# Kernel tuning notes

Hardware: AMD Instinct MI355X
Metric: run time of the kernel (lower is better)

Reference implementation:

```python
import jax, jax.numpy as jnp
import numpy as np

B = 128
NCOL, NCOND = 128, 16
C = NCOL * NCOND          # 2048 channels
NRODT = 512               # groups
D = C // NRODT            # 4 channels per group (tree depth)
NEST = 128                # n_estimator
NFOREST = 100
NHEAD = 1
NHID = 128
EPS = 1e-5


def group_norm(x, w, b, groups, eps=EPS):
    # x: [B, C]; torch GroupNorm (biased variance over each group's channels)
    Bn, Cn = x.shape
    xg = x.reshape(Bn, groups, Cn // groups)
    mu = xg.mean(-1, keepdims=True)
    var = xg.var(-1, keepdims=True)
    xn = ((xg - mu) * jax.lax.rsqrt(var + eps)).reshape(Bn, Cn)
    return xn * w + b


def setup_inputs() -> dict:
    key = jax.random.key(0)
    ks = jax.random.split(key, 11)
    O = jax.random.normal(ks[0], (B, C, 1), jnp.float32)
    gn1_w = jax.random.normal(ks[1], (C,), jnp.float32) * 0.1 + 1.0
    gn1_b = jax.random.normal(ks[2], (C,), jnp.float32) * 0.1
    W1 = jax.random.normal(ks[3], (NRODT, D, D), jnp.float32) * 0.3
    b1 = jax.random.normal(ks[4], (NRODT, D), jnp.float32) * 0.1
    gn2_w = jax.random.normal(ks[5], (C,), jnp.float32) * 0.1 + 1.0
    gn2_b = jax.random.normal(ks[6], (C,), jnp.float32) * 0.1
    W2 = jax.random.normal(ks[7], (NRODT, D, NHEAD), jnp.float32) * 0.3
    b2 = jax.random.normal(ks[8], (NRODT, NHEAD), jnp.float32) * 0.1
    E = jax.random.normal(ks[9], (NRODT, NHID), jnp.float32)
    # eval-mode fixed sample_without_replacement: argsort of uniform, take first NEST
    swr = jnp.argsort(jax.random.uniform(ks[10], (NFOREST, NRODT)), axis=-1)[:, :NEST]
    return {"O": O, "gn1_w": gn1_w, "gn1_b": gn1_b, "W1": W1, "b1": b1,
            "gn2_w": gn2_w, "gn2_b": gn2_b, "W2": W2, "b2": b2, "E": E,
            "swr": swr}


def reference(O, gn1_w, gn1_b, W1, b1, gn2_w, gn2_b, W2, b2, E, swr):
    b = O.shape[0]
    x = O[..., 0]                                    # [B, C]
    # phi_2: GN -> grouped 1x1 conv (per-group DxD matmul) -> ReLU -> GN -> grouped conv to NHEAD
    x = group_norm(x, gn1_w, gn1_b, NRODT)
    x = x.reshape(b, NRODT, D)
    x = jnp.einsum('bgd,gde->bge', x, W1) + b1       # [B, NRODT, D]
    x = jax.nn.relu(x).reshape(b, C)
    x = group_norm(x, gn2_w, gn2_b, NRODT)
    x = x.reshape(b, NRODT, D)
    w = jnp.einsum('bgd,gdh->bgh', x, W2) + b2       # [B, NRODT, NHEAD]
    # gather -> softmax over estimators -> weighted embedding combine
    w_prime = jax.nn.softmax(w[:, swr], axis=-2)[..., None]   # [B, F, EST, H, 1]
    E_prime = E[swr].reshape(1, NFOREST, NEST, NHEAD, NHID // NHEAD)
    F = (w_prime * E_prime).sum(-3).reshape(b, NFOREST, NHID)  # [B, F, NHID]
    return F
```

## Files before the change

### kernel.cpp

```cpp
#include <hip/hip_runtime.h>

#define BB     128
#define CCH    2048
#define NRODT  512
#define NEST   128
#define NF     100
#define NHID   128
#define BT     32
#define TPB    512

typedef __attribute__((ext_vector_type(8))) short short8v;
typedef __attribute__((ext_vector_type(4))) float f32x4;

static __device__ __forceinline__ unsigned short f2bf(float x) {
    unsigned u = __float_as_uint(x);
    u += 0x7FFFu + ((u >> 16) & 1u);
    return (unsigned short)(u >> 16);
}
static __device__ __forceinline__ float bf2f(unsigned short h) {
    return __uint_as_float(((unsigned)h) << 16);
}

__global__ __launch_bounds__(256) void phi2_kernel(
    const float* __restrict__ O,
    const float* __restrict__ g1w, const float* __restrict__ g1b,
    const float* __restrict__ W1,  const float* __restrict__ b1,
    const float* __restrict__ g2w, const float* __restrict__ g2b,
    const float* __restrict__ W2,  const float* __restrict__ b2,
    const float* __restrict__ E,
    float* __restrict__ wbuf,
    unsigned* __restrict__ Esp)
{
    const int t = blockIdx.x * 256 + threadIdx.x;
    const int b = t >> 9;
    const int g = t & (NRODT - 1);

    {
        const float ex = E[t];
        const unsigned short xh = f2bf(ex);
        const float r = ex - bf2f(xh);
        const unsigned short xl = f2bf(r);
        Esp[t] = ((unsigned)xh) | (((unsigned)xl) << 16);
    }

    const float4 x = *reinterpret_cast<const float4*>(O + (size_t)b * CCH + g * 4);

    float m  = 0.25f * ((x.x + x.y) + (x.z + x.w));
    float d0 = x.x - m, d1 = x.y - m, d2 = x.z - m, d3 = x.w - m;
    float v  = 0.25f * ((d0 * d0 + d1 * d1) + (d2 * d2 + d3 * d3));
    float iv = rsqrtf(v + 1e-5f);
    const float4 gw1 = *reinterpret_cast<const float4*>(g1w + g * 4);
    const float4 gb1 = *reinterpret_cast<const float4*>(g1b + g * 4);
    float a0 = fmaf(d0 * iv, gw1.x, gb1.x);
    float a1 = fmaf(d1 * iv, gw1.y, gb1.y);
    float a2 = fmaf(d2 * iv, gw1.z, gb1.z);
    float a3 = fmaf(d3 * iv, gw1.w, gb1.w);

    const float4 r0 = *reinterpret_cast<const float4*>(W1 + g * 16 + 0);
    const float4 r1 = *reinterpret_cast<const float4*>(W1 + g * 16 + 4);
    const float4 r2 = *reinterpret_cast<const float4*>(W1 + g * 16 + 8);
    const float4 r3 = *reinterpret_cast<const float4*>(W1 + g * 16 + 12);
    const float4 bc = *reinterpret_cast<const float4*>(b1 + g * 4);
    float y0 = fmaf(a0, r0.x, fmaf(a1, r1.x, fmaf(a2, r2.x, fmaf(a3, r3.x, bc.x))));
    float y1 = fmaf(a0, r0.y, fmaf(a1, r1.y, fmaf(a2, r2.y, fmaf(a3, r3.y, bc.y))));
    float y2 = fmaf(a0, r0.z, fmaf(a1, r1.z, fmaf(a2, r2.z, fmaf(a3, r3.z, bc.z))));
    float y3 = fmaf(a0, r0.w, fmaf(a1, r1.w, fmaf(a2, r2.w, fmaf(a3, r3.w, bc.w))));
    y0 = fmaxf(y0, 0.f); y1 = fmaxf(y1, 0.f); y2 = fmaxf(y2, 0.f); y3 = fmaxf(y3, 0.f);

    m  = 0.25f * ((y0 + y1) + (y2 + y3));
    d0 = y0 - m; d1 = y1 - m; d2 = y2 - m; d3 = y3 - m;
    v  = 0.25f * ((d0 * d0 + d1 * d1) + (d2 * d2 + d3 * d3));
    iv = rsqrtf(v + 1e-5f);
    const float4 gw2 = *reinterpret_cast<const float4*>(g2w + g * 4);
    const float4 gb2 = *reinterpret_cast<const float4*>(g2b + g * 4);
    float z0 = fmaf(d0 * iv, gw2.x, gb2.x);
    float z1 = fmaf(d1 * iv, gw2.y, gb2.y);
    float z2 = fmaf(d2 * iv, gw2.z, gb2.z);
    float z3 = fmaf(d3 * iv, gw2.w, gb2.w);

    const float4 w2 = *reinterpret_cast<const float4*>(W2 + g * 4);
    float res = fmaf(z0, w2.x, fmaf(z1, w2.y, fmaf(z2, w2.z, fmaf(z3, w2.w, b2[g]))));

    wbuf[g * BB + b] = res;
}

__global__ __launch_bounds__(TPB) void forest_mfma_kernel(
    const float*    __restrict__ wv,
    const unsigned* __restrict__ Esp,
    const int*      __restrict__ swr,
    float* __restrict__ out)
{
    __shared__ __align__(16) short Prow[BT][136];
    __shared__ __align__(16) char  pool[2 * 128 * 72 * 2];
    __shared__ int   ids[NEST];
    __shared__ float invs[BT];

    short (*Ehi)[72] = reinterpret_cast<short(*)[72]>(pool);
    short (*Elo)[72] = reinterpret_cast<short(*)[72]>(pool + 128 * 72 * 2);
    float (*wT)[36]  = reinterpret_cast<float(*)[36]>(pool);

    const int f   = blockIdx.x;
    const int b0  = blockIdx.y * BT;
    const int tid = threadIdx.x;

    if (tid < NEST) ids[tid] = swr[f * NEST + tid];
    __syncthreads();

    {
        const int e = tid >> 2;
        const int j = tid & 3;
        const float* src = wv + (size_t)ids[e] * BB + b0 + (j << 3);
        const float4 va = *reinterpret_cast<const float4*>(src);
        const float4 vb = *reinterpret_cast<const float4*>(src + 4);
        *reinterpret_cast<float4*>(&wT[e][(j << 3) + 0]) = va;
        *reinterpret_cast<float4*>(&wT[e][(j << 3) + 4]) = vb;
    }
    __syncthreads();

    {
        const int bl = tid >> 4;
        const int jj = tid & 15;
        float val[8];
        float mx = -3.4e38f;
        #pragma unroll
        for (int k = 0; k < 8; ++k) {
            val[k] = wT[jj + (k << 4)][bl];
            mx = fmaxf(mx, val[k]);
        }
        mx = fmaxf(mx, __shfl_xor(mx, 1));
        mx = fmaxf(mx, __shfl_xor(mx, 2));
        mx = fmaxf(mx, __shfl_xor(mx, 4));
        mx = fmaxf(mx, __shfl_xor(mx, 8));
        float sum = 0.f;
        #pragma unroll
        for (int k = 0; k < 8; ++k) {
            float ex = __expf(val[k] - mx);
            sum += ex;
            Prow[bl][jj + (k << 4)] = (short)f2bf(ex);
        }
        sum += __shfl_xor(sum, 1);
        sum += __shfl_xor(sum, 2);
        sum += __shfl_xor(sum, 4);
        sum += __shfl_xor(sum, 8);
        if (jj == 0) invs[bl] = 1.f / sum;
    }
    __syncthreads();

    const int lane = tid & 63;
    const int wid  = tid >> 6;
    const int rt   = wid & 1;
    const int ct0  = (wid >> 1) << 1;
    const int lm   = lane & 15;
    const int lk   = (lane >> 4) << 3;

    f32x4 acc0 = {0.f, 0.f, 0.f, 0.f};
    f32x4 acc1 = {0.f, 0.f, 0.f, 0.f};

    const int h  = tid & 127;
    const int eg = tid >> 7;

    #pragma unroll
    for (int hf = 0; hf < 2; ++hf) {
        {
            short hbuf[16], lbuf[16];
            #pragma unroll
            for (int i = 0; i < 16; ++i) {
                const int row = ids[hf * 64 + eg * 16 + i];
                const unsigned v = Esp[(size_t)row * NHID + h];
                hbuf[i] = (short)(v & 0xFFFFu);
                lbuf[i] = (short)(v >> 16);
            }
            if (hf == 1) __syncthreads();
            *reinterpret_cast<short8v*>(&Ehi[h][eg * 16 + 0]) = *reinterpret_cast<short8v*>(&hbuf[0]);
            *reinterpret_cast<short8v*>(&Ehi[h][eg * 16 + 8]) = *reinterpret_cast<short8v*>(&hbuf[8]);
            *reinterpret_cast<short8v*>(&Elo[h][eg * 16 + 0]) = *reinterpret_cast<short8v*>(&lbuf[0]);
            *reinterpret_cast<short8v*>(&Elo[h][eg * 16 + 8]) = *reinterpret_cast<short8v*>(&lbuf[8]);
        }
        __syncthreads();

        #pragma unroll
        for (int kbl = 0; kbl < 2; ++kbl) {
            const short8v a =
                *reinterpret_cast<const short8v*>(&Prow[rt * 16 + lm][(hf * 2 + kbl) * 32 + lk]);
            const short8v bh0 = *reinterpret_cast<const short8v*>(&Ehi[ct0 * 16 + lm][kbl * 32 + lk]);
            const short8v bl0 = *reinterpret_cast<const short8v*>(&Elo[ct0 * 16 + lm][kbl * 32 + lk]);
            const short8v bh1 = *reinterpret_cast<const short8v*>(&Ehi[(ct0 + 1) * 16 + lm][kbl * 32 + lk]);
            const short8v bl1 = *reinterpret_cast<const short8v*>(&Elo[(ct0 + 1) * 16 + lm][kbl * 32 + lk]);
            acc0 = __builtin_amdgcn_mfma_f32_16x16x32_bf16(a, bh0, acc0, 0, 0, 0);
            acc0 = __builtin_amdgcn_mfma_f32_16x16x32_bf16(a, bl0, acc0, 0, 0, 0);
            acc1 = __builtin_amdgcn_mfma_f32_16x16x32_bf16(a, bh1, acc1, 0, 0, 0);
            acc1 = __builtin_amdgcn_mfma_f32_16x16x32_bf16(a, bl1, acc1, 0, 0, 0);
        }
    }

    {
        const size_t stride = (size_t)NF * NHID;
        #pragma unroll
        for (int r = 0; r < 4; ++r) {
            const int row = rt * 16 + ((lane >> 4) << 2) + r;
            const float inv = invs[row];
            float* op = out + (size_t)(b0 + row) * stride + (size_t)f * NHID + lm;
            op[ct0 * 16]       = acc0[r] * inv;
            op[(ct0 + 1) * 16] = acc1[r] * inv;
        }
    }
}

extern "C" void kernel_launch(void* const* d_in, const int* in_sizes, int n_in,
                              void* d_out, int out_size, void* d_ws, size_t ws_size,
                              hipStream_t stream) {
    const float* O   = (const float*)d_in[0];
    const float* g1w = (const float*)d_in[1];
    const float* g1b = (const float*)d_in[2];
    const float* W1  = (const float*)d_in[3];
    const float* b1  = (const float*)d_in[4];
    const float* g2w = (const float*)d_in[5];
    const float* g2b = (const float*)d_in[6];
    const float* W2  = (const float*)d_in[7];
    const float* b2  = (const float*)d_in[8];
    const float* E   = (const float*)d_in[9];
    const int*   swr = (const int*)d_in[10];

    float*    wbuf = (float*)d_ws;
    unsigned* Esp  = (unsigned*)((char*)d_ws + 256 * 1024);
    float*    out  = (float*)d_out;

    phi2_kernel<<<dim3((BB * NRODT) / 256), 256, 0, stream>>>(
        O, g1w, g1b, W1, b1, g2w, g2b, W2, b2, E, wbuf, Esp);

    forest_mfma_kernel<<<dim3(NF, BB / BT), TPB, 0, stream>>>(wbuf, Esp, swr, out);
}
```

Baseline: 16.96 us.

## Prefetch embedding gathers into registers to overlap with softmax and MFMA

Drops the shared-memory index staging and its barrier, reading swr directly from global. The gather of the first half of the E rows is issued at kernel start, alongside the softmax-weight loads. The second half is issued before the first MFMA phase, so global load latency overlaps the softmax and matrix work. This adds 32 live registers per thread for the prefetched values, which may lower occupancy.

```diff
diff --git a/kernel.cpp b/kernel.cpp
--- a/kernel.cpp
+++ b/kernel.cpp
@@ -92,7 +92,6 @@
 {
     __shared__ __align__(16) short Prow[BT][136];
     __shared__ __align__(16) char  pool[2 * 128 * 72 * 2];
-    __shared__ int   ids[NEST];
     __shared__ float invs[BT];
 
     short (*Ehi)[72] = reinterpret_cast<short(*)[72]>(pool);
@@ -102,19 +101,23 @@
     const int f   = blockIdx.x;
     const int b0  = blockIdx.y * BT;
     const int tid = threadIdx.x;
-
-    if (tid < NEST) ids[tid] = swr[f * NEST + tid];
-    __syncthreads();
-
-    {
-        const int e = tid >> 2;
-        const int j = tid & 3;
-        const float* src = wv + (size_t)ids[e] * BB + b0 + (j << 3);
-        const float4 va = *reinterpret_cast<const float4*>(src);
-        const float4 vb = *reinterpret_cast<const float4*>(src + 4);
-        *reinterpret_cast<float4*>(&wT[e][(j << 3) + 0]) = va;
-        *reinterpret_cast<float4*>(&wT[e][(j << 3) + 4]) = vb;
-    }
+    const int* swrf = swr + f * NEST;
+
+    const int e = tid >> 2;
+    const int j = tid & 3;
+    const float* wsrc = wv + (size_t)swrf[e] * BB + b0 + (j << 3);
+    const float4 va = *reinterpret_cast<const float4*>(wsrc);
+    const float4 vb = *reinterpret_cast<const float4*>(wsrc + 4);
+
+    const int h  = tid & 127;
+    const int eg = tid >> 7;
+    unsigned ev0[16];
+    #pragma unroll
+    for (int i = 0; i < 16; ++i)
+        ev0[i] = Esp[(size_t)swrf[eg * 16 + i] * NHID + h];
+
+    *reinterpret_cast<float4*>(&wT[e][(j << 3) + 0]) = va;
+    *reinterpret_cast<float4*>(&wT[e][(j << 3) + 4]) = vb;
     __syncthreads();
 
     {
@@ -144,6 +147,24 @@
         sum += __shfl_xor(sum, 8);
         if (jj == 0) invs[bl] = 1.f / sum;
     }
+    __syncthreads();
+
+    {
+        short hbuf[16], lbuf[16];
+        #pragma unroll
+        for (int i = 0; i < 16; ++i) {
+            hbuf[i] = (short)(ev0[i] & 0xFFFFu);
+            lbuf[i] = (short)(ev0[i] >> 16);
+        }
+        *reinterpret_cast<short8v*>(&Ehi[h][eg * 16 + 0]) = *reinterpret_cast<short8v*>(&hbuf[0]);
+        *reinterpret_cast<short8v*>(&Ehi[h][eg * 16 + 8]) = *reinterpret_cast<short8v*>(&hbuf[8]);
+        *reinterpret_cast<short8v*>(&Elo[h][eg * 16 + 0]) = *reinterpret_cast<short8v*>(&lbuf[0]);
+        *reinterpret_cast<short8v*>(&Elo[h][eg * 16 + 8]) = *reinterpret_cast<short8v*>(&lbuf[8]);
+    }
+    unsigned ev1[16];
+    #pragma unroll
+    for (int i = 0; i < 16; ++i)
+        ev1[i] = Esp[(size_t)swrf[64 + eg * 16 + i] * NHID + h];
     __syncthreads();
 
     const int lane = tid & 63;
@@ -156,41 +177,47 @@
     f32x4 acc0 = {0.f, 0.f, 0.f, 0.f};
     f32x4 acc1 = {0.f, 0.f, 0.f, 0.f};
 
-    const int h  = tid & 127;
-    const int eg = tid >> 7;
-
-    #pragma unroll
-    for (int hf = 0; hf < 2; ++hf) {
-        {
-            short hbuf[16], lbuf[16];
-            #pragma unroll
-            for (int i = 0; i < 16; ++i) {
-                const int row = ids[hf * 64 + eg * 16 + i];
-                const unsigned v = Esp[(size_t)row * NHID + h];
-                hbuf[i] = (short)(v & 0xFFFFu);
-                lbuf[i] = (short)(v >> 16);
-            }
-            if (hf == 1) __syncthreads();
-            *reinterpret_cast<short8v*>(&Ehi[h][eg * 16 + 0]) = *reinterpret_cast<short8v*>(&hbuf[0]);
-            *reinterpret_cast<short8v*>(&Ehi[h][eg * 16 + 8]) = *reinterpret_cast<short8v*>(&hbuf[8]);
-            *reinterpret_cast<short8v*>(&Elo[h][eg * 16 + 0]) = *reinterpret_cast<short8v*>(&lbuf[0]);
-            *reinterpret_cast<short8v*>(&Elo[h][eg * 16 + 8]) = *reinterpret_cast<short8v*>(&lbuf[8]);
-        }
-        __syncthreads();
-
-        #pragma unroll
-        for (int kbl = 0; kbl < 2; ++kbl) {
-            const short8v a =
-                *reinterpret_cast<const short8v*>(&Prow[rt * 16 + lm][(hf * 2 + kbl) * 32 + lk]);
-            const short8v bh0 = *reinterpret_cast<const short8v*>(&Ehi[ct0 * 16 + lm][kbl * 32 + lk]);
-            const short8v bl0 = *reinterpret_cast<const short8v*>(&Elo[ct0 * 16 + lm][kbl * 32 + lk]);
-            const short8v bh1 = *reinterpret_cast<const short8v*>(&Ehi[(ct0 + 1) * 16 + lm][kbl * 32 + lk]);
-            const short8v bl1 = *reinterpret_cast<const short8v*>(&Elo[(ct0 + 1) * 16 + lm][kbl * 32 + lk]);
-            acc0 = __builtin_amdgcn_mfma_f32_16x16x32_bf16(a, bh0, acc0, 0, 0, 0);
-            acc0 = __builtin_amdgcn_mfma_f32_16x16x32_bf16(a, bl0, acc0, 0, 0, 0);
-            acc1 = __builtin_amdgcn_mfma_f32_16x16x32_bf16(a, bh1, acc1, 0, 0, 0);
-            acc1 = __builtin_amdgcn_mfma_f32_16x16x32_bf16(a, bl1, acc1, 0, 0, 0);
-        }
+    #pragma unroll
+    for (int kbl = 0; kbl < 2; ++kbl) {
+        const short8v a =
+            *reinterpret_cast<const short8v*>(&Prow[rt * 16 + lm][kbl * 32 + lk]);
+        const short8v bh0 = *reinterpret_cast<const short8v*>(&Ehi[ct0 * 16 + lm][kbl * 32 + lk]);
+        const short8v bl0 = *reinterpret_cast<const short8v*>(&Elo[ct0 * 16 + lm][kbl * 32 + lk]);
+        const short8v bh1 = *reinterpret_cast<const short8v*>(&Ehi[(ct0 + 1) * 16 + lm][kbl * 32 + lk]);
+        const short8v bl1 = *reinterpret_cast<const short8v*>(&Elo[(ct0 + 1) * 16 + lm][kbl * 32 + lk]);
+        acc0 = __builtin_amdgcn_mfma_f32_16x16x32_bf16(a, bh0, acc0, 0, 0, 0);
+        acc0 = __builtin_amdgcn_mfma_f32_16x16x32_bf16(a, bl0, acc0, 0, 0, 0);
+        acc1 = __builtin_amdgcn_mfma_f32_16x16x32_bf16(a, bh1, acc1, 0, 0, 0);
+        acc1 = __builtin_amdgcn_mfma_f32_16x16x32_bf16(a, bl1, acc1, 0, 0, 0);
+    }
+    __syncthreads();
+
+    {
+        short hbuf[16], lbuf[16];
+        #pragma unroll
+        for (int i = 0; i < 16; ++i) {
+            hbuf[i] = (short)(ev1[i] & 0xFFFFu);
+            lbuf[i] = (short)(ev1[i] >> 16);
+        }
+        *reinterpret_cast<short8v*>(&Ehi[h][eg * 16 + 0]) = *reinterpret_cast<short8v*>(&hbuf[0]);
+        *reinterpret_cast<short8v*>(&Ehi[h][eg * 16 + 8]) = *reinterpret_cast<short8v*>(&hbuf[8]);
+        *reinterpret_cast<short8v*>(&Elo[h][eg * 16 + 0]) = *reinterpret_cast<short8v*>(&lbuf[0]);
+        *reinterpret_cast<short8v*>(&Elo[h][eg * 16 + 8]) = *reinterpret_cast<short8v*>(&lbuf[8]);
+    }
+    __syncthreads();
+
+    #pragma unroll
+    for (int kbl = 0; kbl < 2; ++kbl) {
+        const short8v a =
+            *reinterpret_cast<const short8v*>(&Prow[rt * 16 + lm][(2 + kbl) * 32 + lk]);
+        const short8v bh0 = *reinterpret_cast<const short8v*>(&Ehi[ct0 * 16 + lm][kbl * 32 + lk]);
+        const short8v bl0 = *reinterpret_cast<const short8v*>(&Elo[ct0 * 16 + lm][kbl * 32 + lk]);
+        const short8v bh1 = *reinterpret_cast<const short8v*>(&Ehi[(ct0 + 1) * 16 + lm][kbl * 32 + lk]);
+        const short8v bl1 = *reinterpret_cast<const short8v*>(&Elo[(ct0 + 1) * 16 + lm][kbl * 32 + lk]);
+        acc0 = __builtin_amdgcn_mfma_f32_16x16x32_bf16(a, bh0, acc0, 0, 0, 0);
+        acc0 = __builtin_amdgcn_mfma_f32_16x16x32_bf16(a, bl0, acc0, 0, 0, 0);
+        acc1 = __builtin_amdgcn_mfma_f32_16x16x32_bf16(a, bh1, acc1, 0, 0, 0);
+        acc1 = __builtin_amdgcn_mfma_f32_16x16x32_bf16(a, bl1, acc1, 0, 0, 0);
     }
 
     {
```

Result: no change. 17.21 us (+1.5%).
